# Optimization experiments

Measured on AMD Instinct MI355X. Metric: run time of the kernel, lower is better.

## Reference

```python
import jax, jax.numpy as jnp
import numpy as np
from jax import lax

ID_LEN = 207
INPUT_DIM = 64
OUTPUT_DIM = 128
WIN = 3
BZ = 16
SEQLEN = 64
N_NODES = BZ * ID_LEN          # 3312
N_EDGES = N_NODES * 16         # 52992


def setup_inputs() -> dict:
    key = jax.random.key(0)
    ks = jax.random.split(key, 8)
    x = jax.random.normal(ks[0], (BZ, SEQLEN, ID_LEN * INPUT_DIM), dtype=jnp.float32)
    edge_src = jax.random.randint(ks[1], (N_EDGES,), 0, N_NODES)
    edge_dst = jax.random.randint(ks[2], (N_EDGES,), 0, N_NODES)
    # learned params (q/k weights init N(0, 0.01), zero bias; conv has no bias)
    Wq = 0.01 * jax.random.normal(ks[3], (INPUT_DIM, OUTPUT_DIM), dtype=jnp.float32)
    bq = jnp.zeros((OUTPUT_DIM,), dtype=jnp.float32)
    Wk = 0.01 * jax.random.normal(ks[4], (INPUT_DIM, OUTPUT_DIM), dtype=jnp.float32)
    bk = jnp.zeros((OUTPUT_DIM,), dtype=jnp.float32)
    fan_in = ID_LEN * INPUT_DIM * WIN
    bound = 1.0 / np.sqrt(fan_in)
    conv_w = jax.random.uniform(ks[5], (OUTPUT_DIM, ID_LEN * INPUT_DIM, WIN),
                                minval=-bound, maxval=bound, dtype=jnp.float32)
    return {"x": x, "Wq": Wq, "bq": bq, "Wk": Wk, "bk": bk,
            "conv_w": conv_w, "edge_src": edge_src, "edge_dst": edge_dst}


def _forward(x, Wq, bq, Wk, bk, conv_w, edge_src, edge_dst):
    bz, seqlen, _ = x.shape
    # (bz, seqlen, id_len, d) -> (bz*id_len, seqlen, d)
    xr = x.reshape(bz, seqlen, ID_LEN, INPUT_DIM).transpose(0, 2, 1, 3)
    xr = xr.reshape(-1, seqlen, INPUT_DIM)
    mean_x = xr.mean(axis=1)                       # [N, d]
    q = (mean_x @ Wq + bq) / jnp.sqrt(jnp.float32(OUTPUT_DIM))
    k = mean_x @ Wk + bk
    v = xr.reshape(-1, seqlen * INPUT_DIM)         # [N, seqlen*d]
    N = v.shape[0]
    # per-edge attention score: k[src] . q[dst]
    scores = jnp.sum(k[edge_src] * q[edge_dst], axis=-1)      # [E]
    # segment softmax over incoming edges per dst
    seg_max = jax.ops.segment_max(scores, edge_dst, num_segments=N)
    e = jnp.exp(scores - seg_max[edge_dst])
    denom = jax.ops.segment_sum(e, edge_dst, num_segments=N)
    alpha = e / denom[edge_dst]                                 # [E]
    # weighted gather-sum of big value vectors
    out = jax.ops.segment_sum(alpha[:, None] * v[edge_src], edge_dst, num_segments=N)
    # back to (bz, seqlen, id_len*d)
    y = out.reshape(bz, ID_LEN, seqlen, INPUT_DIM).transpose(0, 2, 1, 3)
    y = y.reshape(bz, seqlen, ID_LEN * INPUT_DIM)
    # Conv1d same padding, no bias: NCH layout
    y = lax.conv_general_dilated(
        y.transpose(0, 2, 1), conv_w, window_strides=(1,), padding="SAME",
        dimension_numbers=("NCH", "OIH", "NCH"))
    return y.transpose(0, 2, 1)                    # [bz, seqlen, output_dim]


def reference(x, Wq, bq, Wk, bk, conv_w, edge_src, edge_dst):
    return _forward(x, Wq, bq, Wk, bk, conv_w, edge_src, edge_dst)
```

## Files before the change

### kernel.cpp

```cpp
#include <hip/hip_runtime.h>
#include <hip/hip_bf16.h>
#include <math.h>

#define BZ 16
#define SEQ 64
#define CID 207
#define DIN 64
#define OCN 128
#define NN (BZ*CID)
#define NE (NN*16)
#define ICD (CID*DIN)
#define KW 3
#define NKPAD 416
#define NKC 32
#define KSPC 13
#define XTOT ((size_t)BZ*SEQ*ICD)
#define TCH 8
#define NCHUNK (SEQ/TCH)
#define CAP 64
#define WFSTEP (3*8*64*8)

#define CVB 832
#define SCB 207
#define WPB (NKPAD*4)

typedef __attribute__((ext_vector_type(8))) short bf16x8;
typedef __attribute__((ext_vector_type(4))) float f32x4;
typedef unsigned short u16;
typedef unsigned int u32;

__device__ __forceinline__ float bflo(u32 u) {
    u32 v = u << 16;
    return __builtin_bit_cast(float, v);
}
__device__ __forceinline__ float bfhi(u32 u) {
    u32 v = u & 0xFFFF0000u;
    return __builtin_bit_cast(float, v);
}
__device__ __forceinline__ u16 f2bf(float f) {
    __hip_bfloat16 h = __float2bfloat16(f);
    return __builtin_bit_cast(u16, h);
}
__device__ __forceinline__ u32 packbf(float f0, float f1) {
    return ((u32)f2bf(f1) << 16) | (u32)f2bf(f0);
}
__device__ __forceinline__ void fma8(float* acc, float a, uint4 v) {
    acc[0] += a * bflo(v.x); acc[1] += a * bfhi(v.x);
    acc[2] += a * bflo(v.y); acc[3] += a * bfhi(v.y);
    acc[4] += a * bflo(v.z); acc[5] += a * bfhi(v.z);
    acc[6] += a * bflo(v.w); acc[7] += a * bfhi(v.w);
}

__global__ __launch_bounds__(256) void zero_kernel(int* __restrict__ p, int n) {
    int i = threadIdx.x;
    for (; i < n; i += 256) p[i] = 0;
}

__global__ __launch_bounds__(256) void k1_kernel(const float* __restrict__ x,
                                                 u16* __restrict__ xt,
                                                 float* __restrict__ meanp,
                                                 const int* __restrict__ esrc,
                                                 const int* __restrict__ edst,
                                                 int* __restrict__ fill,
                                                 int* __restrict__ csr,
                                                 const float* __restrict__ cw,
                                                 u16* __restrict__ wf) {
    __shared__ float s_cw[32][100];
    int bid = blockIdx.x;
    int tid = threadIdx.x;
    if (bid < CVB) {
        int bb = bid / 52;
        int rem = bid - bb * 52;
        int cg = rem >> 2;
        int tq = rem & 3;
        int cl = tid >> 4;
        int dq = (tid & 15) << 2;
        int c = cg * 16 + cl;
        if (c >= CID) return;
        int n = bb * CID + c;
        const float* px = x + (size_t)bb * SEQ * ICD + (size_t)(tq * 16) * ICD + (size_t)c * DIN + dq;
        u16* pxt = xt + ((size_t)(tq * 16) * NN + n) * DIN + dq;
        float ax = 0.f, ay = 0.f, az = 0.f, aw = 0.f;
        #pragma unroll 4
        for (int t = 0; t < 16; ++t) {
            float4 v = *(const float4*)(px + (size_t)t * ICD);
            ax += v.x; ay += v.y; az += v.z; aw += v.w;
            uint2 w2;
            w2.x = packbf(v.x, v.y);
            w2.y = packbf(v.z, v.w);
            *(uint2*)(pxt + (size_t)t * NN * DIN) = w2;
        }
        *(float4*)(meanp + ((size_t)tq * NN + n) * DIN + dq) = make_float4(ax, ay, az, aw);
    } else if (bid < CVB + SCB) {
        int e = (bid - CVB) * 256 + tid;
        int d0 = edst[e];
        int pos = atomicAdd(&fill[d0], 1);
        if (pos < CAP) csr[(d0 << 6) + pos] = esrc[e];
    } else {
        int wkb = bid - (CVB + SCB);
        int kstep = wkb >> 2;
        int p = wkb & 3;
        int ic0 = kstep * 32;
        int col0 = ic0 * 3;
        {
            int oc_l = tid >> 3;
            int seg = tid & 7;
            const float* src = cw + (size_t)(p * 32 + oc_l) * (ICD * KW) + col0 + seg * 12;
            #pragma unroll
            for (int uu = 0; uu < 12; ++uu) {
                int col = seg * 12 + uu;
                float v = (col0 + col < ICD * 3) ? src[uu] : 0.f;
                s_cw[oc_l][col] = v;
            }
        }
        __syncthreads();
        #pragma unroll
        for (int r = 0; r < 2; ++r) {
            int f = tid + 256 * r;
            if (f < 384) {
                int lane = f & 63;
                int g = f >> 6;
                int ntl = g & 1;
                int w = g >> 1;
                int nt = p * 2 + ntl;
                int row = ntl * 16 + (lane & 15);
                int cb = 8 * (lane >> 4);
                uint4 o;
                u32 pk[4];
                #pragma unroll
                for (int pj = 0; pj < 4; ++pj) {
                    float v0 = s_cw[row][(cb + 2 * pj) * 3 + w];
                    float v1 = s_cw[row][(cb + 2 * pj + 1) * 3 + w];
                    pk[pj] = packbf(v0, v1);
                }
                o.x = pk[0]; o.y = pk[1]; o.z = pk[2]; o.w = pk[3];
                size_t off = (((size_t)(kstep * 3 + w) * 8 + nt) * 64 + lane) * 8;
                *(uint4*)(wf + off) = o;
            }
        }
    }
}

__global__ __launch_bounds__(256) void qk_kernel(const float* __restrict__ meanp,
                                                 const float* __restrict__ Wq,
                                                 const float* __restrict__ bq,
                                                 const float* __restrict__ Wk,
                                                 const float* __restrict__ bk,
                                                 float* __restrict__ q,
                                                 float* __restrict__ k) {
    __shared__ float ms[16][DIN];
    int n0 = blockIdx.x * 16;
    int tid = threadIdx.x;
    const size_t PS = (size_t)NN * DIN;
    for (int i = tid; i < 16 * DIN; i += 256) {
        size_t off = (size_t)(n0 + (i >> 6)) * DIN + (i & 63);
        float s = meanp[off] + meanp[PS + off] + meanp[2 * PS + off] + meanp[3 * PS + off];
        ms[i >> 6][i & 63] = s * (1.0f / SEQ);
    }
    __syncthreads();
    int j = tid & 127;
    int g = tid >> 7;
    float accq[8], acck[8];
    float bqv = bq[j], bkv = bk[j];
    #pragma unroll
    for (int r = 0; r < 8; ++r) { accq[r] = bqv; acck[r] = bkv; }
    for (int d = 0; d < DIN; ++d) {
        float wq = Wq[d * OCN + j], wk = Wk[d * OCN + j];
        #pragma unroll
        for (int r = 0; r < 8; ++r) {
            float mv = ms[g * 8 + r][d];
            accq[r] += mv * wq;
            acck[r] += mv * wk;
        }
    }
    const float qscale = 0.088388347648318447f;
    #pragma unroll
    for (int r = 0; r < 8; ++r) {
        int nn = n0 + g * 8 + r;
        q[(size_t)nn * OCN + j] = accq[r] * qscale;
        k[(size_t)nn * OCN + j] = acck[r];
    }
}

__global__ __launch_bounds__(256) void alpha_kernel(const float* __restrict__ q,
                                                    const float* __restrict__ k,
                                                    const int* __restrict__ fill,
                                                    const int* __restrict__ csr,
                                                    float* __restrict__ alpha) {
    __shared__ float qs[OCN];
    __shared__ float sc[CAP];
    __shared__ int sidx[CAP];
    int n = blockIdx.x;
    int deg = fill[n];
    if (deg > CAP) deg = CAP;
    int start = n << 6;
    int tid = threadIdx.x;
    if (tid < OCN) qs[tid] = q[(size_t)n * OCN + tid];
    if (tid < deg) sidx[tid] = csr[start + tid];
    __syncthreads();
    int lane = tid & 63;
    int wv = tid >> 6;
    for (int i = wv; i < deg; i += 4) {
        const float* kk = k + (size_t)sidx[i] * OCN;
        float p = kk[lane] * qs[lane] + kk[lane + 64] * qs[lane + 64];
        #pragma unroll
        for (int off = 32; off; off >>= 1) p += __shfl_down(p, off);
        if (lane == 0) sc[i] = p;
    }
    __syncthreads();
    float m = -1e30f;
    for (int i = 0; i < deg; ++i) m = fmaxf(m, sc[i]);
    __syncthreads();
    if (tid < deg) sc[tid] = __expf(sc[tid] - m);
    __syncthreads();
    float ssum = 0.f;
    for (int i = 0; i < deg; ++i) ssum += sc[i];
    float inv = (deg > 0) ? (1.0f / ssum) : 0.f;
    if (tid < deg) alpha[start + tid] = sc[tid] * inv;
}

__global__ __launch_bounds__(256) void gather2_kernel(const u16* __restrict__ xt,
                                                      const float* __restrict__ alpha,
                                                      const int* __restrict__ fill,
                                                      const int* __restrict__ csr,
                                                      u16* __restrict__ yb) {
    int bid = blockIdx.x;
    int ch = bid & 7;
    int ng = bid >> 3;
    int wid = threadIdx.x >> 6;
    int lane = threadIdx.x & 63;
    int n0 = ng * 16 + wid * 4;
    int t0 = ch * TCH;
    int t = lane >> 3;
    int dg = lane & 7;
    const u16* xbase = xt + ((size_t)(t0 + t) * NN) * DIN + (dg << 3);

    int bb[4], cc[4];
    int sL[4]; float aL[4];
    int mx = 0;
    #pragma unroll
    for (int j = 0; j < 4; ++j) {
        int n = n0 + j;
        bb[j] = n / CID; cc[j] = n - bb[j] * CID;
        int deg = fill[n]; if (deg > CAP) deg = CAP;
        int st = n << 6;
        sL[j] = 0; aL[j] = 0.f;
        if (lane < deg) { sL[j] = csr[st + lane] << 6; aL[j] = alpha[st + lane]; }
        mx = (deg > mx) ? deg : mx;
    }

    float acc[4][8];
    #pragma unroll
    for (int j = 0; j < 4; ++j)
        #pragma unroll
        for (int d = 0; d < 8; ++d) acc[j][d] = 0.f;

    if (mx > 0) {
        float a0[4]; uint4 v0[4];
        #pragma unroll
        for (int j = 0; j < 4; ++j) {
            a0[j] = __shfl(aL[j], 0);
            v0[j] = *(const uint4*)(xbase + __shfl(sL[j], 0));
        }
        for (int i = 1; i < mx; ++i) {
            float a1[4]; uint4 v1[4];
            #pragma unroll
            for (int j = 0; j < 4; ++j) {
                a1[j] = __shfl(aL[j], i);
                v1[j] = *(const uint4*)(xbase + __shfl(sL[j], i));
            }
            #pragma unroll
            for (int j = 0; j < 4; ++j) {
                fma8(acc[j], a0[j], v0[j]);
                a0[j] = a1[j]; v0[j] = v1[j];
            }
        }
        #pragma unroll
        for (int j = 0; j < 4; ++j) fma8(acc[j], a0[j], v0[j]);
    }
    #pragma unroll
    for (int j = 0; j < 4; ++j) {
        uint4 o;
        o.x = packbf(acc[j][0], acc[j][1]);
        o.y = packbf(acc[j][2], acc[j][3]);
        o.z = packbf(acc[j][4], acc[j][5]);
        o.w = packbf(acc[j][6], acc[j][7]);
        *(uint4*)(yb + ((size_t)bb[j] * SEQ + t0 + t) * ICD + cc[j] * DIN + (dg << 3)) = o;
    }
}

__global__ __launch_bounds__(256) void conv_kernel(const u16* __restrict__ yb,
                                                   const u16* __restrict__ wf,
                                                   float* __restrict__ partial) {
    int bid = blockIdx.x;
    int xcd = bid & 7;
    int rest = bid >> 3;
    int th = rest & 1;
    int khi = (rest >> 1) & 3;
    int b = rest >> 3;
    int kc = xcd + (khi << 3);
    int tid = threadIdx.x;
    int lane = tid & 63;
    int wid = tid >> 6;
    int nh = wid >> 1;
    int lrow = lane & 15;
    int lq = lane >> 4;
    int tbase = th * 32 + (wid & 1) * 16;

    f32x4 acc[4];
    #pragma unroll
    for (int n = 0; n < 4; ++n) acc[n] = (f32x4){0.f, 0.f, 0.f, 0.f};

    const u16* ybA = yb + (size_t)b * SEQ * ICD + lq * 8;
    const u16* wfL = wf + (size_t)lane * 8 + ((size_t)nh * 4 * 64) * 8;
    int ks0 = kc * KSPC;

    bf16x8 aA[3], bA[12], aB[3], bB[12];

#define LOAD_AB(aR, bR, KS) do {                                              \
    int kstep_ = ks0 + (KS);                                                  \
    int ic0_ = kstep_ * 32;                                                   \
    _Pragma("unroll")                                                         \
    for (int w_ = 0; w_ < 3; ++w_) {                                          \
        int ts_ = tbase + lrow + w_ - 1;                                      \
        bf16x8 av_ = {0, 0, 0, 0, 0, 0, 0, 0};                                \
        if ((unsigned)ts_ < SEQ)                                              \
            av_ = *(const bf16x8*)(ybA + (size_t)ts_ * ICD + ic0_);           \
        aR[w_] = av_;                                                         \
    }                                                                         \
    const u16* wfp_ = wfL + (size_t)kstep_ * WFSTEP;                          \
    _Pragma("unroll")                                                         \
    for (int w_ = 0; w_ < 3; ++w_) {                                          \
        _Pragma("unroll")                                                     \
        for (int n_ = 0; n_ < 4; ++n_)                                        \
            bR[w_ * 4 + n_] = *(const bf16x8*)(wfp_ + (size_t)((w_ * 8 + n_) * 64) * 8); \
    }                                                                         \
} while (0)

#define COMPUTE(aR, bR) do {                                                  \
    _Pragma("unroll")                                                         \
    for (int w_ = 0; w_ < 3; ++w_) {                                          \
        _Pragma("unroll")                                                     \
        for (int n_ = 0; n_ < 4; ++n_)                                        \
            acc[n_] = __builtin_amdgcn_mfma_f32_16x16x32_bf16(                \
                aR[w_], bR[w_ * 4 + n_], acc[n_], 0, 0, 0);                   \
    }                                                                         \
} while (0)

    LOAD_AB(aA, bA, 0);
    #pragma unroll
    for (int ks = 0; ks < KSPC - 1; ks += 2) {
        LOAD_AB(aB, bB, ks + 1);
        COMPUTE(aA, bA);
        LOAD_AB(aA, bA, ks + 2);
        COMPUTE(aB, bB);
    }
    COMPUTE(aA, bA);

    float* pp = partial + (size_t)kc * ((size_t)BZ * SEQ * OCN) + (size_t)b * SEQ * OCN + nh * 64;
    #pragma unroll
    for (int n = 0; n < 4; ++n) {
        #pragma unroll
        for (int r = 0; r < 4; ++r) {
            int t = tbase + lq * 4 + r;
            pp[(size_t)t * OCN + n * 16 + lrow] = acc[n][r];
        }
    }
#undef LOAD_AB
#undef COMPUTE
}

__global__ __launch_bounds__(256) void reduce_kernel(const float* __restrict__ partial,
                                                     float* __restrict__ out) {
    int i = (blockIdx.x * 256 + threadIdx.x) * 4;
    float4 s = make_float4(0.f, 0.f, 0.f, 0.f);
    #pragma unroll
    for (int kc = 0; kc < NKC; ++kc) {
        float4 v = *(const float4*)(partial + (size_t)kc * 131072 + i);
        s.x += v.x; s.y += v.y; s.z += v.z; s.w += v.w;
    }
    *(float4*)(out + i) = s;
}

extern "C" void kernel_launch(void* const* d_in, const int* in_sizes, int n_in,
                              void* d_out, int out_size, void* d_ws, size_t ws_size,
                              hipStream_t stream) {
    const float* x   = (const float*)d_in[0];
    const float* Wq  = (const float*)d_in[1];
    const float* bqv = (const float*)d_in[2];
    const float* Wk  = (const float*)d_in[3];
    const float* bkv = (const float*)d_in[4];
    const float* cw  = (const float*)d_in[5];
    const int* esrc  = (const int*)d_in[6];
    const int* edst  = (const int*)d_in[7];

    char* ws = (char*)d_ws;
    size_t o = 0;
    auto alloc = [&](size_t bytes) {
        void* p = ws + o;
        o += (bytes + 255) & ~(size_t)255;
        return p;
    };
    u16*   xt    = (u16*)alloc(XTOT * 2);
    u16*   yb    = (u16*)alloc(XTOT * 2);
    u16*   wf    = (u16*)alloc((size_t)NKPAD * 3 * 8 * 64 * 8 * 2);
    float* meanp = (float*)alloc((size_t)4 * NN * DIN * 4);
    float* q     = (float*)alloc((size_t)NN * OCN * 4);
    float* k     = (float*)alloc((size_t)NN * OCN * 4);
    int*   fill  = (int*)alloc((size_t)NN * 4);
    int*   csr   = (int*)alloc((size_t)NN * CAP * 4);
    float* alpha = (float*)alloc((size_t)NN * CAP * 4);
    float* partial = (float*)xt;

    zero_kernel<<<dim3(1), dim3(256), 0, stream>>>(fill, NN);
    k1_kernel<<<dim3(CVB + SCB + WPB), dim3(256), 0, stream>>>(x, xt, meanp, esrc, edst, fill, csr, cw, wf);
    qk_kernel<<<dim3(NN / 16), dim3(256), 0, stream>>>(meanp, Wq, bqv, Wk, bkv, q, k);
    alpha_kernel<<<dim3(NN), dim3(256), 0, stream>>>(q, k, fill, csr, alpha);
    gather2_kernel<<<dim3((NN / 16) * NCHUNK), dim3(256), 0, stream>>>(xt, alpha, fill, csr, yb);
    conv_kernel<<<dim3(1024), dim3(256), 0, stream>>>(yb, wf, partial);
    reduce_kernel<<<dim3(131072 / 4 / 256), dim3(256), 0, stream>>>(partial, (float*)d_out);
}
```

Baseline: 133.6 us.

## Give each conv warp all 64 timesteps to reuse weight fragments

Each warp in the conv kernel now computes all four 16-row time tiles for one batch instead of a single tile, so every weight fragment loaded is reused across four MFMA tiles. Block mapping changes so each block covers two batches, and the grid shrinks from 1024 to 256 blocks. This cuts redundant weight loads from global/L2, but raises register pressure (64 accumulator vectors plus doubled A buffers) and lowers parallelism to one block per CU.

```diff
diff --git a/kernel.cpp b/kernel.cpp
--- a/kernel.cpp
+++ b/kernel.cpp
@@ -295,38 +295,42 @@
     int bid = blockIdx.x;
     int xcd = bid & 7;
     int rest = bid >> 3;
-    int th = rest & 1;
-    int khi = (rest >> 1) & 3;
-    int b = rest >> 3;
+    int khi = rest & 3;
+    int bp = rest >> 2;
     int kc = xcd + (khi << 3);
     int tid = threadIdx.x;
     int lane = tid & 63;
     int wid = tid >> 6;
+    int b = bp * 2 + (wid & 1);
     int nh = wid >> 1;
     int lrow = lane & 15;
     int lq = lane >> 4;
-    int tbase = th * 32 + (wid & 1) * 16;
-
-    f32x4 acc[4];
-    #pragma unroll
-    for (int n = 0; n < 4; ++n) acc[n] = (f32x4){0.f, 0.f, 0.f, 0.f};
+
+    f32x4 acc[4][4];
+    #pragma unroll
+    for (int tt = 0; tt < 4; ++tt)
+        #pragma unroll
+        for (int n = 0; n < 4; ++n) acc[tt][n] = (f32x4){0.f, 0.f, 0.f, 0.f};
 
     const u16* ybA = yb + (size_t)b * SEQ * ICD + lq * 8;
     const u16* wfL = wf + (size_t)lane * 8 + ((size_t)nh * 4 * 64) * 8;
     int ks0 = kc * KSPC;
 
-    bf16x8 aA[3], bA[12], aB[3], bB[12];
+    bf16x8 aA[12], bA[12], aB[12], bB[12];
 
 #define LOAD_AB(aR, bR, KS) do {                                              \
     int kstep_ = ks0 + (KS);                                                  \
     int ic0_ = kstep_ * 32;                                                   \
     _Pragma("unroll")                                                         \
-    for (int w_ = 0; w_ < 3; ++w_) {                                          \
-        int ts_ = tbase + lrow + w_ - 1;                                      \
-        bf16x8 av_ = {0, 0, 0, 0, 0, 0, 0, 0};                                \
-        if ((unsigned)ts_ < SEQ)                                              \
-            av_ = *(const bf16x8*)(ybA + (size_t)ts_ * ICD + ic0_);           \
-        aR[w_] = av_;                                                         \
+    for (int tt_ = 0; tt_ < 4; ++tt_) {                                       \
+        _Pragma("unroll")                                                     \
+        for (int w_ = 0; w_ < 3; ++w_) {                                      \
+            int ts_ = tt_ * 16 + lrow + w_ - 1;                               \
+            bf16x8 av_ = {0, 0, 0, 0, 0, 0, 0, 0};                            \
+            if ((unsigned)ts_ < SEQ)                                          \
+                av_ = *(const bf16x8*)(ybA + (size_t)ts_ * ICD + ic0_);       \
+            aR[tt_ * 3 + w_] = av_;                                           \
+        }                                                                     \
     }                                                                         \
     const u16* wfp_ = wfL + (size_t)kstep_ * WFSTEP;                          \
     _Pragma("unroll")                                                         \
@@ -341,9 +345,12 @@
     _Pragma("unroll")                                                         \
     for (int w_ = 0; w_ < 3; ++w_) {                                          \
         _Pragma("unroll")                                                     \
-        for (int n_ = 0; n_ < 4; ++n_)                                        \
-            acc[n_] = __builtin_amdgcn_mfma_f32_16x16x32_bf16(                \
-                aR[w_], bR[w_ * 4 + n_], acc[n_], 0, 0, 0);                   \
+        for (int tt_ = 0; tt_ < 4; ++tt_) {                                   \
+            _Pragma("unroll")                                                 \
+            for (int n_ = 0; n_ < 4; ++n_)                                    \
+                acc[tt_][n_] = __builtin_amdgcn_mfma_f32_16x16x32_bf16(       \
+                    aR[tt_ * 3 + w_], bR[w_ * 4 + n_], acc[tt_][n_], 0, 0, 0);\
+        }                                                                     \
     }                                                                         \
 } while (0)
 
@@ -359,11 +366,14 @@
 
     float* pp = partial + (size_t)kc * ((size_t)BZ * SEQ * OCN) + (size_t)b * SEQ * OCN + nh * 64;
     #pragma unroll
-    for (int n = 0; n < 4; ++n) {
-        #pragma unroll
-        for (int r = 0; r < 4; ++r) {
-            int t = tbase + lq * 4 + r;
-            pp[(size_t)t * OCN + n * 16 + lrow] = acc[n][r];
+    for (int tt = 0; tt < 4; ++tt) {
+        #pragma unroll
+        for (int n = 0; n < 4; ++n) {
+            #pragma unroll
+            for (int r = 0; r < 4; ++r) {
+                int t = tt * 16 + lq * 4 + r;
+                pp[(size_t)t * OCN + n * 16 + lrow] = acc[tt][n][r];
+            }
         }
     }
 #undef LOAD_AB
@@ -417,6 +427,6 @@
     qk_kernel<<<dim3(NN / 16), dim3(256), 0, stream>>>(meanp, Wq, bqv, Wk, bkv, q, k);
     alpha_kernel<<<dim3(NN), dim3(256), 0, stream>>>(q, k, fill, csr, alpha);
     gather2_kernel<<<dim3((NN / 16) * NCHUNK), dim3(256), 0, stream>>>(xt, alpha, fill, csr, yb);
-    conv_kernel<<<dim3(1024), dim3(256), 0, stream>>>(yb, wf, partial);
+    conv_kernel<<<dim3(256), dim3(256), 0, stream>>>(yb, wf, partial);
     reduce_kernel<<<dim3(131072 / 4 / 256), dim3(256), 0, stream>>>(partial, (float*)d_out);
 }
```

New measurement: 121.7 us. 8.9% less time.
